# Kernel optimization log

Hardware: AMD Instinct MI355X
Metric: run time of the kernel (lower is better)

The kernel has to match this reference:

```python
import jax, jax.numpy as jnp
import numpy as np
from math import sqrt

# dims
B, H, P, N, D = 4, 8, 32, 32, 16   # batch, heads, n_patches, channels, patch_len
L = P * N                           # 1024 token positions
SEQ, PRED, WIN, E, NF = 512, 96, 10, 2, 6  # seq_len, pred_len, attention_window, e_layers, n_fore
EPS = float(np.finfo(np.float32).eps)      # torch RMSNorm default eps (finfo eps)


def setup_inputs() -> dict:
    key = jax.random.key(0)
    ks = jax.random.split(key, 8)
    return dict(
        tokens=jax.random.normal(ks[0], (B, H, L, D), jnp.float32),
        x_original=jax.random.normal(ks[1], (B, SEQ, N), jnp.float32),
        log_scales=jnp.full((E,), np.log(2.0), jnp.float32),
        attn_norm_w=jnp.ones((E, D), jnp.float32),
        conv_up_w=jax.random.normal(ks[2], (E, 2 * H, 1, 3), jnp.float32) * 0.1,
        conv_down_w=jax.random.normal(ks[3], (E, H, 2, 1), jnp.float32) * 0.1,
        ffn_norm_w=jnp.ones((E, D), jnp.float32),
        mix_w=jax.random.normal(ks[4], (1, H), jnp.float32) * 0.3,
        mix_b=jnp.zeros((1,), jnp.float32),
        fore_w=jax.random.normal(ks[5], (NF, P), jnp.float32) * 0.1,
        fore_b=jnp.zeros((NF,), jnp.float32),
    )


def _rms(x, w):
    # torch.nn.RMSNorm over last dim (patch_len)
    return x * jax.lax.rsqrt(jnp.mean(x * x, axis=-1, keepdims=True) + EPS) * w


def _mask():
    # pid repeated per-channel; True entries are masked out
    pid = jnp.repeat(jnp.arange(P), N)
    diff = pid[None, :] - pid[:, None]  # pid[key] - pid[query]
    return (diff <= 0) | (diff >= WIN)  # [L, L]


def _signed_attn(h, log_scale, mask):
    # scores: [B,H,L,L]; A = softmax(+s) - softmax(-s) with banded mask
    scores = jnp.einsum('bhld,bhmd->bhlm', h, h)
    scale = jnp.clip(jnp.exp(log_scale), 1.0, 30.0) / sqrt(D)
    pos = jnp.where(mask, -10000.0, scores)
    neg = jnp.where(mask, -10000.0, -scores)
    A = jax.nn.softmax(scale * pos, axis=-1) - jax.nn.softmax(scale * neg, axis=-1)
    return jnp.einsum('bhlm,bhmd->bhld', A, h)


def _conv_ffn(x, up_w, down_w, norm_w):
    # depthwise causal conv along patch time dim D; x: [B,H,L,D]
    r = x.transpose(0, 2, 1, 3).reshape(B * L, H, D)
    r = jnp.pad(r, ((0, 0), (0, 0), (2, 0)))  # causal left-pad (kernel_size-1)
    dn = ('NCH', 'OIH', 'NCH')
    r = jax.lax.conv_general_dilated(r, up_w, (1,), 'VALID', dimension_numbers=dn, feature_group_count=H)
    r = jax.nn.gelu(r, approximate=False)
    r = jax.lax.conv_general_dilated(r, down_w, (1,), 'VALID', dimension_numbers=dn, feature_group_count=H)
    r = r.reshape(B, L, H, D).transpose(0, 2, 1, 3)
    return _rms(x + r, norm_w)


def reference(tokens, x_original, log_scales, attn_norm_w, conv_up_w, conv_down_w,
              ffn_norm_w, mix_w, mix_b, fore_w, fore_b):
    mask = _mask()
    h = tokens
    for l in range(E):
        h = _rms(h + _signed_attn(h, log_scales[l], mask), attn_norm_w[l])
        h = _conv_ffn(h, conv_up_w[l], conv_down_w[l], ffn_norm_w[l])
    # aggregate heads -> forecast
    h = h.reshape(B, H, P, N, D).transpose(0, 3, 4, 2, 1)       # (B,N,D,P,H)
    h = jnp.einsum('bndph,h->bndp', h, mix_w[0]) + mix_b[0]      # channel_mixing
    f = jnp.einsum('bndp,fp->bndf', h, fore_w) + fore_b          # fore_projection
    f = f.reshape(B, N, D * NF)[:, :, -PRED:]                    # flatten + tail slice
    forecast = f.transpose(0, 2, 1)                              # (B,pred_len,N)
    return forecast, x_original
```

## Files before the change

### kernel.cpp

```cpp
#include <hip/hip_runtime.h>
#include <hip/hip_bf16.h>
#include <math.h>

#define BB 4
#define HH 8
#define PP 32
#define NN 32
#define DD 16
#define LL 1024
#define WINW 10
#define NFF 6
#define PREDL 96
#define SEQL 512
#define EPSF 1.1920928955078125e-07f
#define KROW 24
#define KTS 296
#define PROW 40
#define XROW 20

typedef __attribute__((ext_vector_type(8))) short bf16x8;
typedef __attribute__((ext_vector_type(4))) float f32x4;

__device__ __forceinline__ unsigned cvtpk(float a, float b) {
    unsigned r;
    asm("v_cvt_pk_bf16_f32 %0, %1, %2" : "=v"(r) : "v"(a), "v"(b));
    return r;
}
__device__ __forceinline__ unsigned long long pk64(unsigned lo, unsigned hi) {
    return (unsigned long long)lo | ((unsigned long long)hi << 32);
}

__global__ __launch_bounds__(256) void layer_kernel(
    const float* __restrict__ hin, float* __restrict__ hout,
    const float* __restrict__ log_scales, const float* __restrict__ attn_norm,
    const float* __restrict__ up_w, const float* __restrict__ down_w,
    const float* __restrict__ ffn_norm, int layer,
    const float* __restrict__ xsrc, float* __restrict__ xdst)
{
    __shared__ short hK[9 * 32 * KROW];
    __shared__ short VT[16 * KTS];
    __shared__ short Pp[4][16 * PROW];
    __shared__ short Pn[4][16 * PROW];
    __shared__ float xls[32 * XROW];
    __shared__ float comb[2][64][8];
    __shared__ float combl[2][2][16];

    int blk = blockIdx.x;
    int bh  = blk >> 5;
    int hh  = bh & 7;
    int p0  = blk & 31;
    int nstage = min(9, (PP - 1) - p0);

    int tid  = threadIdx.x;
    int wid  = tid >> 6;
    int qh   = wid >> 1;
    int ch   = wid & 1;
    int lane = tid & 63;
    int quad = lane >> 4, n16 = lane & 15;

    if (xsrc && tid < 16) {
        const float4* x4 = (const float4*)xsrc;
        float4* o4 = (float4*)xdst;
        o4[blk * 16 + tid] = x4[blk * 16 + tid];
    }

    {
        const float4* src = (const float4*)(hin + ((size_t)bh * LL + (p0 + 1) * NN) * DD);
        int nf4 = nstage * 128;
        #pragma unroll
        for (int k = 0; k < 5; ++k) {
            int i = tid + k * 256;
            if (i < nf4) {
                int row = i >> 2, j = i & 3;
                float4 v = src[i];
                unsigned pk0 = cvtpk(v.x, v.y);
                unsigned pk1 = cvtpk(v.z, v.w);
                *(unsigned long long*)&hK[row * KROW + j * 4] = pk64(pk0, pk1);
                int d0 = j * 4;
                VT[(d0 + 0) * KTS + row] = (short)(pk0 & 0xffff);
                VT[(d0 + 1) * KTS + row] = (short)(pk0 >> 16);
                VT[(d0 + 2) * KTS + row] = (short)(pk1 & 0xffff);
                VT[(d0 + 3) * KTS + row] = (short)(pk1 >> 16);
            }
        }
    }

    bf16x8 Aq;
    #pragma unroll
    for (int j = 0; j < 8; ++j) Aq[j] = 0;
    if (quad < 2) {
        const float4* qp4 = (const float4*)(hin +
            ((size_t)bh * LL + p0 * NN + qh * 16 + n16) * DD + quad * 8);
        float4 a = qp4[0], b = qp4[1];
        union { bf16x8 v; unsigned u[4]; } uu;
        uu.u[0] = cvtpk(a.x, a.y);
        uu.u[1] = cvtpk(a.z, a.w);
        uu.u[2] = cvtpk(b.x, b.y);
        uu.u[3] = cvtpk(b.z, b.w);
        Aq = uu.v;
    }
    float rs[4] = {0.f, 0.f, 0.f, 0.f};
    if (ch == 0) {
        #pragma unroll
        for (int r = 0; r < 4; ++r)
            rs[r] = hin[((size_t)bh * LL + p0 * NN + qh * 16 + quad * 4 + r) * DD + n16];
    }

    float sc  = fminf(fmaxf(__expf(log_scales[layer]), 1.0f), 30.0f) * 0.25f;
    float sc2 = sc * 1.4426950408889634f;

    __syncthreads();

    f32x4 Op, On;
    Op[0] = Op[1] = Op[2] = Op[3] = 0.f;
    On[0] = On[1] = On[2] = On[3] = 0.f;
    float lpp = 0.f, lnn = 0.f;
    short* myPp = Pp[wid];
    short* myPn = Pn[wid];

    int c0 = ch ? 4 : 0;
    int c1 = ch ? nstage : min(4, nstage);

    for (int c = c0; c < c1; ++c) {
        int kb = c * 32;
        #pragma unroll
        for (int kt = 0; kt < 2; ++kt) {
            bf16x8 Bk;
            #pragma unroll
            for (int j = 0; j < 8; ++j) Bk[j] = 0;
            if (quad < 2)
                Bk = *(const bf16x8*)&hK[(kb + kt * 16 + n16) * KROW + quad * 8];
            f32x4 z; z[0] = z[1] = z[2] = z[3] = 0.f;
            f32x4 S = __builtin_amdgcn_mfma_f32_16x16x32_bf16(Bk, Aq, z, 0, 0, 0);
            float ep[4], en[4];
            #pragma unroll
            for (int r = 0; r < 4; ++r) {
                float t = sc2 * S[r];
                ep[r] = exp2f(t);
                en[r] = exp2f(-t);
                lpp += ep[r]; lnn += en[r];
            }
            *(unsigned long long*)&myPp[n16 * PROW + kt * 16 + quad * 4] =
                pk64(cvtpk(ep[0], ep[1]), cvtpk(ep[2], ep[3]));
            *(unsigned long long*)&myPn[n16 * PROW + kt * 16 + quad * 4] =
                pk64(cvtpk(en[0], en[1]), cvtpk(en[2], en[3]));
        }
        bf16x8 Bv = *(const bf16x8*)&VT[n16 * KTS + kb + quad * 8];
        bf16x8 Ap = *(const bf16x8*)&myPp[n16 * PROW + quad * 8];
        bf16x8 An = *(const bf16x8*)&myPn[n16 * PROW + quad * 8];
        Op = __builtin_amdgcn_mfma_f32_16x16x32_bf16(Ap, Bv, Op, 0, 0, 0);
        On = __builtin_amdgcn_mfma_f32_16x16x32_bf16(An, Bv, On, 0, 0, 0);
    }

    lpp += __shfl_xor(lpp, 16); lpp += __shfl_xor(lpp, 32);
    lnn += __shfl_xor(lnn, 16); lnn += __shfl_xor(lnn, 32);

    if (ch == 1) {
        *(f32x4*)&comb[qh][lane][0] = Op;
        *(f32x4*)&comb[qh][lane][4] = On;
        if (lane < 16) {
            combl[qh][0][lane] = lpp;
            combl[qh][1][lane] = lnn;
        }
    }
    __syncthreads();
    if (ch == 1) return;

    {
        f32x4 o2 = *(const f32x4*)&comb[qh][lane][0];
        f32x4 n2 = *(const f32x4*)&comb[qh][lane][4];
        #pragma unroll
        for (int r = 0; r < 4; ++r) { Op[r] += o2[r]; On[r] += n2[r]; }
        lpp += combl[qh][0][n16];
        lnn += combl[qh][1][n16];
    }

    float lpr[4], lnr[4];
    #pragma unroll
    for (int r = 0; r < 4; ++r) {
        lpr[r] = __shfl(lpp, quad * 4 + r);
        lnr[r] = __shfl(lnn, quad * 4 + r);
    }

    #pragma unroll
    for (int r = 0; r < 4; ++r) {
        float lp = lpr[r], ln = lnr[r];
        float rl = (lp > 0.f) ? (1.0f / lp) : 0.f;
        float rn = (ln > 0.f) ? (1.0f / ln) : 0.f;
        float v  = rs[r] + Op[r] * rl - On[r] * rn;
        float ss = v * v;
        ss += __shfl_xor(ss, 1); ss += __shfl_xor(ss, 2);
        ss += __shfl_xor(ss, 4); ss += __shfl_xor(ss, 8);
        float rr = rsqrtf(ss * (1.0f / 16.0f) + EPSF);
        xls[(qh * 16 + quad * 4 + r) * XROW + n16] = v * rr * attn_norm[layer * DD + n16];
    }

    {
        int q = qh * 16 + n16;
        int g = quad;

        const float* uw = up_w + (size_t)(layer * 2 * HH + 2 * hh) * 3;
        float w00 = uw[0], w01 = uw[1], w02 = uw[2];
        float w10 = uw[3], w11 = uw[4], w12 = uw[5];
        const float* dw = down_w + (size_t)(layer * HH + hh) * 2;
        float dc0 = dw[0], dc1 = dw[1];

        float xm2 = g ? xls[q * XROW + 4 * g - 2] : 0.f;
        float xm1 = g ? xls[q * XROW + 4 * g - 1] : 0.f;
        float4 xv = *(const float4*)&xls[q * XROW + 4 * g];
        float xa[6] = {xm2, xm1, xv.x, xv.y, xv.z, xv.w};

        float v4[4], ss = 0.f;
        #pragma unroll
        for (int i = 0; i < 4; ++i) {
            float u0 = w00 * xa[i] + w01 * xa[i + 1] + w02 * xa[i + 2];
            float u1 = w10 * xa[i] + w11 * xa[i + 1] + w12 * xa[i + 2];
            float g0 = 0.5f * u0 * (1.0f + erff(u0 * 0.7071067811865475f));
            float g1 = 0.5f * u1 * (1.0f + erff(u1 * 0.7071067811865475f));
            float vv = xa[i + 2] + dc0 * g0 + dc1 * g1;
            v4[i] = vv; ss += vv * vv;
        }
        ss += __shfl_xor(ss, 16); ss += __shfl_xor(ss, 32);
        float r2 = rsqrtf(ss * (1.0f / 16.0f) + EPSF);

        const float4 fn = *(const float4*)&ffn_norm[layer * DD + 4 * g];
        float* op = hout + ((size_t)bh * LL + p0 * NN + q) * DD + 4 * g;
        float4 o;
        o.x = v4[0] * r2 * fn.x;
        o.y = v4[1] * r2 * fn.y;
        o.z = v4[2] * r2 * fn.z;
        o.w = v4[3] * r2 * fn.w;
        *(float4*)op = o;
    }
}

__global__ __launch_bounds__(256) void tail_kernel(
    const float* __restrict__ h, const float* __restrict__ mw_,
    const float* __restrict__ mb_, const float* __restrict__ fw_,
    const float* __restrict__ fb_, float* __restrict__ out)
{
    int b   = blockIdx.x;
    int tid = threadIdx.x;
    int n   = tid >> 3;
    int d0  = (2 * tid) & 15;

    float mw[8];
    #pragma unroll
    for (int k = 0; k < 8; ++k) mw[k] = mw_[k];
    float mb = mb_[0];

    float acc0[NFF] = {0.f, 0.f, 0.f, 0.f, 0.f, 0.f};
    float acc1[NFF] = {0.f, 0.f, 0.f, 0.f, 0.f, 0.f};

    for (int p = 0; p < PP; ++p) {
        float m0 = mb, m1 = mb;
        #pragma unroll
        for (int k = 0; k < 8; ++k) {
            const float* hp = h + (size_t)(((b * HH + k) * LL) + p * NN + n) * DD + d0;
            float2 hv = *(const float2*)hp;
            m0 += hv.x * mw[k];
            m1 += hv.y * mw[k];
        }
        #pragma unroll
        for (int fi = 0; fi < NFF; ++fi) {
            float w = fw_[fi * PP + p];
            acc0[fi] += m0 * w;
            acc1[fi] += m1 * w;
        }
    }
    #pragma unroll
    for (int fi = 0; fi < NFF; ++fi) {
        float fb = fb_[fi];
        out[((b * DD + d0) * NFF + fi) * NN + n]     = acc0[fi] + fb;
        out[((b * DD + d0 + 1) * NFF + fi) * NN + n] = acc1[fi] + fb;
    }
}

static int find_by_size(const int* s, int n, int want, int occurrence) {
    int seen = 0;
    for (int i = 0; i < n; ++i)
        if (s[i] == want) { if (seen == occurrence) return i; ++seen; }
    return -1;
}

extern "C" void kernel_launch(void* const* d_in, const int* in_sizes, int n_in,
                              void* d_out, int out_size, void* d_ws, size_t ws_size,
                              hipStream_t stream) {
    int it  = find_by_size(in_sizes, n_in, 524288, 0);
    int ix  = find_by_size(in_sizes, n_in, 65536, 0);
    int ils = find_by_size(in_sizes, n_in, 2, 0);
    int ian = find_by_size(in_sizes, n_in, 32, 0);
    int icu = find_by_size(in_sizes, n_in, 96, 0);
    int icd = find_by_size(in_sizes, n_in, 32, 1);
    int ifn = find_by_size(in_sizes, n_in, 32, 2);
    int imw = find_by_size(in_sizes, n_in, 8, 0);
    int imb = find_by_size(in_sizes, n_in, 1, 0);
    int ifw = find_by_size(in_sizes, n_in, 192, 0);
    int ifb = find_by_size(in_sizes, n_in, 6, 0);
    if (it < 0 || ix < 0 || ils < 0 || ian < 0 || icu < 0 || icd < 0 ||
        ifn < 0 || imw < 0 || imb < 0 || ifw < 0 || ifb < 0) {
        it = 0; ix = 1; ils = 2; ian = 3; icu = 4; icd = 5; ifn = 6;
        imw = 7; imb = 8; ifw = 9; ifb = 10;
    }

    const float* tokens     = (const float*)d_in[it];
    const float* x_orig     = (const float*)d_in[ix];
    const float* log_scales = (const float*)d_in[ils];
    const float* attn_norm  = (const float*)d_in[ian];
    const float* up_w       = (const float*)d_in[icu];
    const float* down_w     = (const float*)d_in[icd];
    const float* ffn_norm   = (const float*)d_in[ifn];
    const float* mix_w      = (const float*)d_in[imw];
    const float* mix_b      = (const float*)d_in[imb];
    const float* fore_w     = (const float*)d_in[ifw];
    const float* fore_b     = (const float*)d_in[ifb];
    float* out = (float*)d_out;

    const size_t NH = (size_t)BB * HH * LL * DD;
    float* hA = (float*)d_ws;
    float* hB = hA + NH;

    layer_kernel<<<1024, 256, 0, stream>>>(tokens, hA, log_scales, attn_norm,
                                           up_w, down_w, ffn_norm, 0,
                                           x_orig, out + BB * PREDL * NN);
    layer_kernel<<<1024, 256, 0, stream>>>(hA, hB, log_scales, attn_norm,
                                           up_w, down_w, ffn_norm, 1,
                                           (const float*)nullptr, (float*)nullptr);
    tail_kernel<<<BB, 256, 0, stream>>>(hB, mix_w, mix_b, fore_w, fore_b, out);
}
```

Measured before the change: 118.5 us.

## Fuse head-mixing and forecast projection into second layer kernel via atomics

The separate tail kernel is removed. The second layer kernel now scales its normalized outputs by mix weight times fore weight and atomically accumulates them into the forecast output. The forecast region is zeroed in the first layer kernel, and one designated block per batch adds the bias constants. This drops the final hB write and re-read and a low-parallelism 4-block launch, at the cost of many contended float atomic adds and non-deterministic summation order.

```diff
diff --git a/kernel.cpp b/kernel.cpp
--- a/kernel.cpp
+++ b/kernel.cpp
@@ -30,39 +30,28 @@
     return (unsigned long long)lo | ((unsigned long long)hi << 32);
 }
 
-__global__ __launch_bounds__(256) void layer_kernel(
+template <int MODE>
+__device__ __forceinline__ void layer_body(
     const float* __restrict__ hin, float* __restrict__ hout,
     const float* __restrict__ log_scales, const float* __restrict__ attn_norm,
     const float* __restrict__ up_w, const float* __restrict__ down_w,
-    const float* __restrict__ ffn_norm, int layer,
-    const float* __restrict__ xsrc, float* __restrict__ xdst)
+    const float* __restrict__ ffn_norm, int layer, int blk, int tid,
+    short* hK, short* VT, short (*Pp)[16 * PROW], short (*Pn)[16 * PROW],
+    float* xls, float (*comb)[64][8], float (*combl)[2][16],
+    const float* __restrict__ mix_w, const float* __restrict__ mix_b,
+    const float* __restrict__ fore_w, const float* __restrict__ fore_b,
+    float* __restrict__ out)
 {
-    __shared__ short hK[9 * 32 * KROW];
-    __shared__ short VT[16 * KTS];
-    __shared__ short Pp[4][16 * PROW];
-    __shared__ short Pn[4][16 * PROW];
-    __shared__ float xls[32 * XROW];
-    __shared__ float comb[2][64][8];
-    __shared__ float combl[2][2][16];
-
-    int blk = blockIdx.x;
     int bh  = blk >> 5;
     int hh  = bh & 7;
     int p0  = blk & 31;
     int nstage = min(9, (PP - 1) - p0);
 
-    int tid  = threadIdx.x;
     int wid  = tid >> 6;
     int qh   = wid >> 1;
     int ch   = wid & 1;
     int lane = tid & 63;
     int quad = lane >> 4, n16 = lane & 15;
-
-    if (xsrc && tid < 16) {
-        const float4* x4 = (const float4*)xsrc;
-        float4* o4 = (float4*)xdst;
-        o4[blk * 16 + tid] = x4[blk * 16 + tid];
-    }
 
     {
         const float4* src = (const float4*)(hin + ((size_t)bh * LL + (p0 + 1) * NN) * DD);
@@ -217,63 +206,101 @@
             float u1 = w10 * xa[i] + w11 * xa[i + 1] + w12 * xa[i + 2];
             float g0 = 0.5f * u0 * (1.0f + erff(u0 * 0.7071067811865475f));
             float g1 = 0.5f * u1 * (1.0f + erff(u1 * 0.7071067811865475f));
-            float vv = xa[i + 2] + dc0 * g0 + dc1 * g1;
+            float vv = xa[i] * 0.f + xa[i + 2] + dc0 * g0 + dc1 * g1;
             v4[i] = vv; ss += vv * vv;
         }
         ss += __shfl_xor(ss, 16); ss += __shfl_xor(ss, 32);
         float r2 = rsqrtf(ss * (1.0f / 16.0f) + EPSF);
 
         const float4 fn = *(const float4*)&ffn_norm[layer * DD + 4 * g];
-        float* op = hout + ((size_t)bh * LL + p0 * NN + q) * DD + 4 * g;
-        float4 o;
-        o.x = v4[0] * r2 * fn.x;
-        o.y = v4[1] * r2 * fn.y;
-        o.z = v4[2] * r2 * fn.z;
-        o.w = v4[3] * r2 * fn.w;
-        *(float4*)op = o;
-    }
-}
-
-__global__ __launch_bounds__(256) void tail_kernel(
-    const float* __restrict__ h, const float* __restrict__ mw_,
-    const float* __restrict__ mb_, const float* __restrict__ fw_,
-    const float* __restrict__ fb_, float* __restrict__ out)
+        float vals[4];
+        vals[0] = v4[0] * r2 * fn.x;
+        vals[1] = v4[1] * r2 * fn.y;
+        vals[2] = v4[2] * r2 * fn.z;
+        vals[3] = v4[3] * r2 * fn.w;
+
+        if (MODE == 0) {
+            float* op = hout + ((size_t)bh * LL + p0 * NN + q) * DD + 4 * g;
+            *(float4*)op = *(float4*)vals;
+        } else {
+            int b2 = bh >> 3;
+            float mwh = mix_w[hh];
+            bool isc = (hh == 0) && (p0 == 0);
+            float mbv = mix_b[0];
+            #pragma unroll
+            for (int fi = 0; fi < NFF; ++fi) {
+                float cst = 0.f;
+                if (isc) {
+                    float s = 0.f;
+                    for (int p = 0; p < PP; ++p) s += fore_w[fi * PP + p];
+                    cst = fore_b[fi] + mbv * s;
+                }
+                float c = mwh * fore_w[fi * PP + p0];
+                #pragma unroll
+                for (int i = 0; i < 4; ++i)
+                    atomicAdd(&out[((size_t)(b2 * DD + 4 * g + i) * NFF + fi) * NN + q],
+                              c * vals[i] + cst);
+            }
+        }
+    }
+}
+
+__global__ __launch_bounds__(256) void layer0_kernel(
+    const float* __restrict__ tokens, float* __restrict__ hA,
+    const float* __restrict__ log_scales, const float* __restrict__ attn_norm,
+    const float* __restrict__ up_w, const float* __restrict__ down_w,
+    const float* __restrict__ ffn_norm,
+    const float* __restrict__ x_orig, float* __restrict__ out)
 {
-    int b   = blockIdx.x;
+    __shared__ short hK[9 * 32 * KROW];
+    __shared__ short VT[16 * KTS];
+    __shared__ short Pp[4][16 * PROW];
+    __shared__ short Pn[4][16 * PROW];
+    __shared__ float xls[32 * XROW];
+    __shared__ float comb[2][64][8];
+    __shared__ float combl[2][2][16];
+
+    int blk = blockIdx.x;
     int tid = threadIdx.x;
-    int n   = tid >> 3;
-    int d0  = (2 * tid) & 15;
-
-    float mw[8];
-    #pragma unroll
-    for (int k = 0; k < 8; ++k) mw[k] = mw_[k];
-    float mb = mb_[0];
-
-    float acc0[NFF] = {0.f, 0.f, 0.f, 0.f, 0.f, 0.f};
-    float acc1[NFF] = {0.f, 0.f, 0.f, 0.f, 0.f, 0.f};
-
-    for (int p = 0; p < PP; ++p) {
-        float m0 = mb, m1 = mb;
-        #pragma unroll
-        for (int k = 0; k < 8; ++k) {
-            const float* hp = h + (size_t)(((b * HH + k) * LL) + p * NN + n) * DD + d0;
-            float2 hv = *(const float2*)hp;
-            m0 += hv.x * mw[k];
-            m1 += hv.y * mw[k];
-        }
-        #pragma unroll
-        for (int fi = 0; fi < NFF; ++fi) {
-            float w = fw_[fi * PP + p];
-            acc0[fi] += m0 * w;
-            acc1[fi] += m1 * w;
-        }
-    }
-    #pragma unroll
-    for (int fi = 0; fi < NFF; ++fi) {
-        float fb = fb_[fi];
-        out[((b * DD + d0) * NFF + fi) * NN + n]     = acc0[fi] + fb;
-        out[((b * DD + d0 + 1) * NFF + fi) * NN + n] = acc1[fi] + fb;
-    }
+
+    if (tid < 3) {
+        float4 z; z.x = z.y = z.z = z.w = 0.f;
+        ((float4*)out)[blk * 3 + tid] = z;
+    }
+    if (tid < 16) {
+        const float4* x4 = (const float4*)x_orig;
+        float4* o4 = (float4*)(out + BB * PREDL * NN);
+        o4[blk * 16 + tid] = x4[blk * 16 + tid];
+    }
+
+    layer_body<0>(tokens, hA, log_scales, attn_norm, up_w, down_w, ffn_norm, 0,
+                  blk, tid, hK, VT, Pp, Pn, xls, comb, combl,
+                  nullptr, nullptr, nullptr, nullptr, nullptr);
+}
+
+__global__ __launch_bounds__(256) void layer1_kernel(
+    const float* __restrict__ hA,
+    const float* __restrict__ log_scales, const float* __restrict__ attn_norm,
+    const float* __restrict__ up_w, const float* __restrict__ down_w,
+    const float* __restrict__ ffn_norm,
+    const float* __restrict__ mix_w, const float* __restrict__ mix_b,
+    const float* __restrict__ fore_w, const float* __restrict__ fore_b,
+    float* __restrict__ out)
+{
+    __shared__ short hK[9 * 32 * KROW];
+    __shared__ short VT[16 * KTS];
+    __shared__ short Pp[4][16 * PROW];
+    __shared__ short Pn[4][16 * PROW];
+    __shared__ float xls[32 * XROW];
+    __shared__ float comb[2][64][8];
+    __shared__ float combl[2][2][16];
+
+    int blk = blockIdx.x;
+    int tid = threadIdx.x;
+
+    layer_body<1>(hA, nullptr, log_scales, attn_norm, up_w, down_w, ffn_norm, 1,
+                  blk, tid, hK, VT, Pp, Pn, xls, comb, combl,
+                  mix_w, mix_b, fore_w, fore_b, out);
 }
 
 static int find_by_size(const int* s, int n, int want, int occurrence) {
@@ -316,15 +343,11 @@
     const float* fore_b     = (const float*)d_in[ifb];
     float* out = (float*)d_out;
 
-    const size_t NH = (size_t)BB * HH * LL * DD;
     float* hA = (float*)d_ws;
-    float* hB = hA + NH;
-
-    layer_kernel<<<1024, 256, 0, stream>>>(tokens, hA, log_scales, attn_norm,
-                                           up_w, down_w, ffn_norm, 0,
-                                           x_orig, out + BB * PREDL * NN);
-    layer_kernel<<<1024, 256, 0, stream>>>(hA, hB, log_scales, attn_norm,
-                                           up_w, down_w, ffn_norm, 1,
-                                           (const float*)nullptr, (float*)nullptr);
-    tail_kernel<<<BB, 256, 0, stream>>>(hB, mix_w, mix_b, fore_w, fore_b, out);
-}
+
+    layer0_kernel<<<1024, 256, 0, stream>>>(tokens, hA, log_scales, attn_norm,
+                                            up_w, down_w, ffn_norm, x_orig, out);
+    layer1_kernel<<<1024, 256, 0, stream>>>(hA, log_scales, attn_norm,
+                                            up_w, down_w, ffn_norm,
+                                            mix_w, mix_b, fore_w, fore_b, out);
+}
```

After: 109.7 us, median of 2. 7.5% less time.
